# Performance work log

Hardware: AMD Instinct MI355X
Metric: run time of the kernel (lower is better)

## Reference

```python
import jax, jax.numpy as jnp
import numpy as np


def reference(x, phi, sigma, M_phi_plus, M_phi_minus, M_u, padded_sl):
    """STU forward: spectral FFT convolution + autoregressive input term.

    x:   (B, L, D) input sequence
    phi: (L, K) time-domain spectral filters (top-K Hankel eigenvectors);
         V = rfft(phi, n=padded_sl) matches the module's precomputed V.
    sigma: (K,) Hankel eigenvalues
    M_phi_plus/minus: (K, D, D) per-filter projections
    M_u: (k_u, D, D) AR-on-input matrices
    """
    B, L, D = x.shape
    K = sigma.shape[0]
    n = padded_sl  # FFT length for causal linear convolution

    # Alternating-sign trick for the 'minus' featurization:
    # sum_j (-1)^j phi_j u_{t-j} = (-1)^t * conv(phi, sgn*u)_t
    sgn = jnp.where(jnp.arange(L) % 2 == 0, 1.0, -1.0).astype(x.dtype)[None, :, None]  # (1,L,1)

    V = jnp.fft.rfft(phi, n=n, axis=0)                       # (n//2+1, K) complex
    U = jnp.fft.rfft(jnp.stack([x, x * sgn], axis=-1), n=n, axis=1)  # (B, n//2+1, D, 2)
    prod = V[None, :, :, None, None] * U[:, :, None, :, :]    # (B, n//2+1, K, D, 2)
    conv = jnp.fft.irfft(prod, n=n, axis=1)[:, :L]            # (B, L, K, D, 2) causal conv
    U_plus = conv[..., 0]
    U_minus = conv[..., 1] * sgn[..., None]                   # undo sign on output side

    # Fold sigma^{1/4} scaling into the projection matrices.
    sig4 = (sigma ** 0.25).astype(x.dtype)[:, None, None]     # (K,1,1)
    spectral = (
        jnp.einsum('blkd,kdo->blo', U_plus, M_phi_plus * sig4)
        + jnp.einsum('blkd,kdo->blo', U_minus, M_phi_minus * sig4)
    )

    # compute_ar_u: y_t += sum_{i=0}^{k_u-1} x_{t-i} @ M_u[i]  (use_ar_u=True)
    ar_u = jnp.einsum('bld,do->blo', x, M_u[0])
    for i in range(1, M_u.shape[0]):  # small fixed depth k_u=3
        x_shift = jnp.pad(x, ((0, 0), (i, 0), (0, 0)))[:, :L]
        ar_u = ar_u + jnp.einsum('bld,do->blo', x_shift, M_u[i])

    # use_ar_y=False branch; dropout=0 (identity)
    return spectral + ar_u


def setup_inputs() -> dict:
    key = jax.random.key(0)
    ks = jax.random.split(key, 6)
    B, L, D, K, KU, N = 1, 2048, 768, 16, 3, 4096
    x = jax.random.normal(ks[0], (B, L, D), jnp.float32)
    phi = jax.random.normal(ks[1], (L, K), jnp.float32) / np.sqrt(L).astype(np.float32)
    sigma = jax.random.uniform(ks[2], (K,), jnp.float32, 0.1, 1.0)
    M_phi_plus = jax.random.normal(ks[3], (K, D, D), jnp.float32) * 0.02
    M_phi_minus = jax.random.normal(ks[4], (K, D, D), jnp.float32) * 0.02
    M_u = jax.random.normal(ks[5], (KU, D, D), jnp.float32) * 0.02
    return {"x": x, "phi": phi, "sigma": sigma, "M_phi_plus": M_phi_plus,
            "M_phi_minus": M_phi_minus, "M_u": M_u, "padded_sl": N}
```

## Files before the change

### kernel.cpp

```cpp
#include <hip/hip_runtime.h>

typedef __attribute__((ext_vector_type(8))) short bf16x8;
typedef __attribute__((ext_vector_type(4))) float f32x4;

#define SL 2048
#define DM 768
#define NCH 32
#define MSPEC 24576
#define MTOT  26880

#define SPLITK 10
#define KSLICE 2688
#define NT 42
#define NITER 21

__device__ __forceinline__ short f2bf(float f) {
  unsigned u = __builtin_bit_cast(unsigned, f);
  u = (u + 0x7FFFu + ((u >> 16) & 1u)) >> 16;
  return (short)u;
}

__device__ __forceinline__ void gload16(const short* g, short* l) {
  __builtin_amdgcn_global_load_lds(
      (const __attribute__((address_space(1))) void*)g,
      (__attribute__((address_space(3))) void*)l, 16, 0, 0);
}


__global__ __launch_bounds__(256) void k_zero(float4* out) {
  out[blockIdx.x * 256 + threadIdx.x] = float4{0.f, 0.f, 0.f, 0.f};
}

__global__ __launch_bounds__(256) void k_prep_xT(const float* __restrict__ x,
                                                 short* __restrict__ xT) {
  __shared__ short tile[64][65];
  const int d0 = blockIdx.x * 64, l0 = blockIdx.y * 64;
  const int t = threadIdx.x;
#pragma unroll
  for (int rr = 0; rr < 16; ++rr) {
    int ll = rr * 4 + (t >> 6), dl = t & 63;
    tile[ll][dl] = f2bf(x[(size_t)(l0 + ll) * DM + d0 + dl]);
  }
  __syncthreads();
#pragma unroll
  for (int rr = 0; rr < 16; ++rr) {
    int dl = rr * 4 + (t >> 6), ll = t & 63;
    xT[(size_t)(d0 + dl) * SL + l0 + ll] = tile[ll][dl];
  }
}

__global__ __launch_bounds__(256) void k_prep_ar(const float* __restrict__ x,
                                                 short* __restrict__ U) {
  int id = blockIdx.x * 256 + threadIdx.x;
  int l = id / DM, d = id - l * DM;
#pragma unroll
  for (int i = 0; i < 3; ++i) {
    short v = 0;
    if (l >= i) v = f2bf(x[(size_t)(l - i) * DM + d]);
    U[(size_t)l * MTOT + MSPEC + i * DM + d] = v;
  }
}

__global__ __launch_bounds__(256) void k_prep_T(const float* __restrict__ phi,
                                                short* __restrict__ Tmat) {
  int idx = blockIdx.x * 256 + threadIdx.x;
  int b = idx & 127, a = (idx >> 7) & 127, dlag = (idx >> 14) & 15, c = idx >> 18;
  int j = dlag * 128 + a - b;
  short v = 0;
  if (j >= 0) {
    float p = phi[j * 16 + (c & 15)];
    if (c >= 16 && (j & 1)) p = -p;
    v = f2bf(p);
  }
  Tmat[idx] = v;
}

__global__ __launch_bounds__(256) void k_prep_M(const float* __restrict__ Mp,
                                                const float* __restrict__ Mm,
                                                const float* __restrict__ Mu,
                                                const float* __restrict__ sigma,
                                                short* __restrict__ McatT) {
  __shared__ short tile[64][65];
  const int m0 = blockIdx.x * 64, o0 = blockIdx.y * 64;
  const int t = threadIdx.x;
#pragma unroll
  for (int rr = 0; rr < 16; ++rr) {
    int ml = rr * 4 + (t >> 6), ol = t & 63;
    int m = m0 + ml, o = o0 + ol;
    float v;
    if (m < MSPEC) {
      int c = m / DM, d = m - c * DM;
      int k = c & 15;
      float s4 = sqrtf(sqrtf(sigma[k]));
      if (c < 16) v = Mp[((size_t)c * DM + d) * DM + o] * s4;
      else        v = Mm[((size_t)(c - 16) * DM + d) * DM + o] * s4;
    } else {
      int mm = m - MSPEC;
      int i = mm / DM, d = mm - i * DM;
      v = Mu[((size_t)i * DM + d) * DM + o];
    }
    tile[ml][ol] = f2bf(v);
  }
  __syncthreads();
#pragma unroll
  for (int rr = 0; rr < 16; ++rr) {
    int ol = rr * 4 + (t >> 6), ml = t & 63;
    McatT[(size_t)(o0 + ol) * MTOT + m0 + ml] = tile[ml][ol];
  }
}

__global__ __launch_bounds__(256) void k_gemm1(const short* __restrict__ Tmat,
                                               const short* __restrict__ xT,
                                               short* __restrict__ U) {
  __shared__ __align__(16) short As[2][128 * 32];
  __shared__ __align__(16) short Bs[2][128 * 32];
  const int wid = blockIdx.x;
  const int xcd = wid & 7;
  const int slot = wid >> 3;
  const int c = xcd * 4 + (slot & 3);
  const int dtile = (slot >> 2) % 6;
  const int ib = 15 - (slot >> 2) / 6;
  const int t = threadIdx.x;
  const int lane = t & 63, wave = t >> 6;
  const int wm = (wave >> 1) * 64, wn = (wave & 1) * 64;
  const int lrow = lane & 15, quad = lane >> 4;
  const int l4 = lane >> 2, lq = lane & 3;
  const int r0 = wave * 32 + l4;
  const int swz = (lq ^ ((l4 >> 1) & 3)) * 8;
  const int foff = ((quad ^ ((lrow >> 1) & 3)) << 3);

  f32x4 acc[4][4] = {};
  const short* Abase = Tmat + ((size_t)(c * 16) << 14) + r0 * 128 + swz;
  const short* Bbase = xT + (size_t)dtile * 128 * SL + (size_t)r0 * SL + swz;
  const int nit = 4 * (ib + 1);

  auto stage = [&](int it, int buf) {
    int dlag = it >> 2, kk = it & 3;
    const short* Ad = Abase + ((size_t)dlag << 14) + kk * 32;
    const short* Bd = Bbase + (ib - dlag) * 128 + kk * 32;
    short* lA = &As[buf][wave * 1024 + lane * 8];
    short* lB = &Bs[buf][wave * 1024 + lane * 8];
    gload16(Ad, lA);
    gload16(Ad + 16 * 128, lA + 512);
    gload16(Bd, lB);
    gload16(Bd + 16 * SL, lB + 512);
  };

  stage(0, 0);
  int cur = 0;
  for (int it = 0; it < nit; ++it) {
    __syncthreads();
    if (it + 1 < nit) stage(it + 1, cur ^ 1);
    bf16x8 af[4], bfr[4];
#pragma unroll
    for (int im = 0; im < 4; ++im)
      af[im] = *reinterpret_cast<const bf16x8*>(&As[cur][(wm + im * 16 + lrow) * 32 + foff]);
#pragma unroll
    for (int in = 0; in < 4; ++in)
      bfr[in] = *reinterpret_cast<const bf16x8*>(&Bs[cur][(wn + in * 16 + lrow) * 32 + foff]);
#pragma unroll
    for (int im = 0; im < 4; ++im)
#pragma unroll
      for (int in = 0; in < 4; ++in)
        acc[im][in] = __builtin_amdgcn_mfma_f32_16x16x32_bf16(af[im], bfr[in], acc[im][in], 0, 0, 0);
    cur ^= 1;
  }
  const int l0 = ib * 128, colbase = c * DM + dtile * 128;
#pragma unroll
  for (int im = 0; im < 4; ++im)
#pragma unroll
    for (int in = 0; in < 4; ++in)
#pragma unroll
      for (int r4 = 0; r4 < 4; ++r4) {
        int row = wm + im * 16 + quad * 4 + r4;
        int col = wn + in * 16 + lrow;
        U[(size_t)(l0 + row) * MTOT + colbase + col] = f2bf(acc[im][in][r4]);
      }
}


#define LDSREADS(BUF, KS, MQ)                                                   \
    _Pragma("unroll")                                                           \
    for (int q_ = 0; q_ < 4; ++q_)                                              \
      af_[q_] = *reinterpret_cast<const bf16x8*>(                               \
          &As[BUF][KS][wm1][((MQ) * 64 + q_ * 16 + lrow) * 32 + foff]);         \
    if ((MQ) == 0) {                                                            \
      _Pragma("unroll")                                                         \
      for (int i_ = 0; i_ < 4; ++i_)                                            \
        bf_[i_] = *reinterpret_cast<const bf16x8*>(                             \
            &Bs[BUF][KS][hB][(rB0 + i_ * 16 + lrow) * 32 + foff]);              \
    }

#define DOMFMA(MQ)                                                              \
    _Pragma("unroll")                                                           \
    for (int q_ = 0; q_ < 4; ++q_)                                              \
      _Pragma("unroll")                                                         \
      for (int i_ = 0; i_ < 4; ++i_)                                            \
        acc[(MQ) * 4 + q_][i_] = __builtin_amdgcn_mfma_f32_16x16x32_bf16(       \
            af_[q_], bf_[i_], acc[(MQ) * 4 + q_][i_], 0, 0, 0)

#define STA(SBUF, SKS, SKT) do { int kt_ = (SKT); if (kt_ < NT) {               \
    const short* g_ = Abase + kt_ * 64 + (SKS) * 32;                            \
    gload16(g_, &As[SBUF][SKS][0][t8]);                                         \
    gload16(g_ + (size_t)128 * MTOT, &As[SBUF][SKS][1][t8]); } } while (0)

#define STB(SBUF, SKS, SKT) do { int kt_ = (SKT); if (kt_ < NT) {               \
    const short* g_ = Bbase + kt_ * 64 + (SKS) * 32;                            \
    gload16(g_, &Bs[SBUF][SKS][0][t8]);                                         \
    gload16(g_ + (size_t)128 * MTOT, &Bs[SBUF][SKS][1][t8]); } } while (0)

#define PHASE(BUF, KS, MQ, VMODE, STG) do {                                     \
    asm volatile("" ::: "memory");            \
    bf16x8 af_[4];                                                              \
    if ((VMODE) == 1) asm volatile("s_waitcnt vmcnt(6)" ::: "memory");          \
    if ((VMODE) == 2) {                                                         \
      if (j < NITER - 1) asm volatile("s_waitcnt vmcnt(6)" ::: "memory");       \
      else               asm volatile("s_waitcnt vmcnt(0)" ::: "memory");       \
    }                                                                           \
    if ((VMODE) == 0) { LDSREADS(BUF, KS, MQ) }                                 \
    STG;                                                                        \
    __builtin_amdgcn_s_barrier();                                               \
    asm volatile("" ::: "memory");                                              \
    if ((VMODE) != 0) { LDSREADS(BUF, KS, MQ) }                                 \
    asm volatile("s_waitcnt lgkmcnt(0)" ::: "memory");                          \
    __builtin_amdgcn_sched_barrier(0);                                          \
    __builtin_amdgcn_s_setprio(1);                                              \
    DOMFMA(MQ);                                                                 \
    __builtin_amdgcn_s_setprio(0);                                              \
    __builtin_amdgcn_s_barrier();                                               \
  } while (0)

__global__ __launch_bounds__(512, 2) void k_gemm2_8p(const short* __restrict__ U,
                                                     const short* __restrict__ McatT,
                                                     float* __restrict__ out) {
  __shared__ __align__(16) short As[2][2][2][4096];
  __shared__ __align__(16) short Bs[2][2][2][4096];
  const int bid = blockIdx.x;
  const int tile = bid % 24, kc = bid / 24;
  const int mt = tile & 7, nt_ = tile >> 3;
  const int m0 = mt * 256, o0 = nt_ * 256;
  const int kbase = kc * KSLICE;
  const int t = threadIdx.x;
  const int lane = t & 63, wave = t >> 6;
  const int wm1 = wave >> 2;
  const int hB = (wave & 3) >> 1;
  const int rB0 = (wave & 1) * 64;
  const int lrow = lane & 15, quad = lane >> 4;
  const int foff = (quad ^ ((lrow >> 1) & 3)) << 3;
  const int r = t >> 2;
  const int cswz = ((t & 3) ^ ((r >> 1) & 3)) << 3;
  const int t8 = t * 8;

  const short* Abase = U     + (size_t)(m0 + r) * MTOT + kbase + cswz;
  const short* Bbase = McatT + (size_t)(o0 + r) * MTOT + kbase + cswz;

  f32x4 acc[8][4] = {};

  STB(0, 0, 0); STA(0, 0, 0); STB(0, 1, 0); STA(0, 1, 0);
  STB(1, 0, 1); STA(1, 0, 1); STB(1, 1, 1);

  for (int j = 0; j < NITER; ++j) {
    bf16x8 bf_[4];
    PHASE(0, 0, 0, 1, STA(1, 1, 2 * j + 1));
    PHASE(0, 0, 1, 0, STB(0, 0, 2 * j + 2));
    PHASE(0, 1, 0, 0, STA(0, 0, 2 * j + 2));
    PHASE(0, 1, 1, 0, STB(0, 1, 2 * j + 2));
    PHASE(1, 0, 0, 2, STA(0, 1, 2 * j + 2));
    PHASE(1, 0, 1, 0, STB(1, 0, 2 * j + 3));
    PHASE(1, 1, 0, 0, STA(1, 0, 2 * j + 3));
    PHASE(1, 1, 1, 0, STB(1, 1, 2 * j + 3));
  }

  const int wm128 = (wave >> 2) * 128, wn64 = (wave & 3) * 64;
#pragma unroll
  for (int im = 0; im < 8; ++im)
#pragma unroll
    for (int in = 0; in < 4; ++in)
#pragma unroll
      for (int r4 = 0; r4 < 4; ++r4) {
        int row = m0 + wm128 + im * 16 + quad * 4 + r4;
        int col = o0 + wn64 + in * 16 + lrow;
        atomicAdd(&out[(size_t)row * DM + col], acc[im][in][r4]);
      }
}

extern "C" void kernel_launch(void* const* d_in, const int* in_sizes, int n_in,
                              void* d_out, int out_size, void* d_ws, size_t ws_size,
                              hipStream_t stream) {
  (void)in_sizes; (void)n_in; (void)out_size; (void)ws_size;
  const float* x     = (const float*)d_in[0];
  const float* phi   = (const float*)d_in[1];
  const float* sigma = (const float*)d_in[2];
  const float* Mp    = (const float*)d_in[3];
  const float* Mm    = (const float*)d_in[4];
  const float* Mu    = (const float*)d_in[5];
  float* out = (float*)d_out;
  char* ws = (char*)d_ws;

  short* U     = (short*)(ws);
  short* Tmat  = (short*)(ws + 110100480);
  short* xT    = (short*)(ws + 126877696);
  short* McatT = (short*)(ws + 130023424);

  k_zero<<<dim3(1536), dim3(256), 0, stream>>>((float4*)out);
  k_prep_xT<<<dim3(12, 32), dim3(256), 0, stream>>>(x, xT);
  k_prep_ar<<<dim3(6144), dim3(256), 0, stream>>>(x, U);
  k_prep_T<<<dim3(32768), dim3(256), 0, stream>>>(phi, Tmat);
  k_prep_M<<<dim3(420, 12), dim3(256), 0, stream>>>(Mp, Mm, Mu, sigma, McatT);
  k_gemm1<<<dim3(3072), dim3(256), 0, stream>>>(Tmat, xT, U);
  k_gemm2_8p<<<dim3(240), dim3(512), 0, stream>>>(U, McatT, out);
}
```

Before: 419.5 us.

## Retile Toeplitz conv GEMM to 256x256 8-phase pipeline; add split-K partial reduce

Replaces the 128x128 Toeplitz-convolution GEMM with a 256x256-tile, 512-thread kernel that reuses the 8-phase software-pipelined schedule of the projection GEMM. It adds a zero block to Tmat so the causal lag lookups near the diagonal can read zeros instead of branching. When the workspace is large enough, the split-K projection GEMM writes per-slice partials and a separate reduction kernel sums them, replacing the zero-fill and float atomics. The cost is extra workspace and extra memory traffic for the partials, plus coarser load balance in the triangular first GEMM.

```diff
diff --git a/kernel.cpp b/kernel.cpp
--- a/kernel.cpp
+++ b/kernel.cpp
@@ -11,8 +11,15 @@
 
 #define SPLITK 10
 #define KSLICE 2688
-#define NT 42
-#define NITER 21
+#define NT2 42
+#define NITER2 21
+
+#define WS_U      0
+#define WS_TMAT   110100480ULL
+#define WS_XT     126910464ULL
+#define WS_MCAT   130056192ULL
+#define WS_PART   171343872ULL
+#define WS_NEED   234258432ULL
 
 __device__ __forceinline__ short f2bf(float f) {
   unsigned u = __builtin_bit_cast(unsigned, f);
@@ -64,7 +71,9 @@
 __global__ __launch_bounds__(256) void k_prep_T(const float* __restrict__ phi,
                                                 short* __restrict__ Tmat) {
   int idx = blockIdx.x * 256 + threadIdx.x;
-  int b = idx & 127, a = (idx >> 7) & 127, dlag = (idx >> 14) & 15, c = idx >> 18;
+  int c = idx >> 18;
+  if (c >= 32) { Tmat[idx] = 0; return; }
+  int b = idx & 127, a = (idx >> 7) & 127, dlag = (idx >> 14) & 15;
   int j = dlag * 128 + a - b;
   short v = 0;
   if (j >= 0) {
@@ -109,75 +118,6 @@
   }
 }
 
-__global__ __launch_bounds__(256) void k_gemm1(const short* __restrict__ Tmat,
-                                               const short* __restrict__ xT,
-                                               short* __restrict__ U) {
-  __shared__ __align__(16) short As[2][128 * 32];
-  __shared__ __align__(16) short Bs[2][128 * 32];
-  const int wid = blockIdx.x;
-  const int xcd = wid & 7;
-  const int slot = wid >> 3;
-  const int c = xcd * 4 + (slot & 3);
-  const int dtile = (slot >> 2) % 6;
-  const int ib = 15 - (slot >> 2) / 6;
-  const int t = threadIdx.x;
-  const int lane = t & 63, wave = t >> 6;
-  const int wm = (wave >> 1) * 64, wn = (wave & 1) * 64;
-  const int lrow = lane & 15, quad = lane >> 4;
-  const int l4 = lane >> 2, lq = lane & 3;
-  const int r0 = wave * 32 + l4;
-  const int swz = (lq ^ ((l4 >> 1) & 3)) * 8;
-  const int foff = ((quad ^ ((lrow >> 1) & 3)) << 3);
-
-  f32x4 acc[4][4] = {};
-  const short* Abase = Tmat + ((size_t)(c * 16) << 14) + r0 * 128 + swz;
-  const short* Bbase = xT + (size_t)dtile * 128 * SL + (size_t)r0 * SL + swz;
-  const int nit = 4 * (ib + 1);
-
-  auto stage = [&](int it, int buf) {
-    int dlag = it >> 2, kk = it & 3;
-    const short* Ad = Abase + ((size_t)dlag << 14) + kk * 32;
-    const short* Bd = Bbase + (ib - dlag) * 128 + kk * 32;
-    short* lA = &As[buf][wave * 1024 + lane * 8];
-    short* lB = &Bs[buf][wave * 1024 + lane * 8];
-    gload16(Ad, lA);
-    gload16(Ad + 16 * 128, lA + 512);
-    gload16(Bd, lB);
-    gload16(Bd + 16 * SL, lB + 512);
-  };
-
-  stage(0, 0);
-  int cur = 0;
-  for (int it = 0; it < nit; ++it) {
-    __syncthreads();
-    if (it + 1 < nit) stage(it + 1, cur ^ 1);
-    bf16x8 af[4], bfr[4];
-#pragma unroll
-    for (int im = 0; im < 4; ++im)
-      af[im] = *reinterpret_cast<const bf16x8*>(&As[cur][(wm + im * 16 + lrow) * 32 + foff]);
-#pragma unroll
-    for (int in = 0; in < 4; ++in)
-      bfr[in] = *reinterpret_cast<const bf16x8*>(&Bs[cur][(wn + in * 16 + lrow) * 32 + foff]);
-#pragma unroll
-    for (int im = 0; im < 4; ++im)
-#pragma unroll
-      for (int in = 0; in < 4; ++in)
-        acc[im][in] = __builtin_amdgcn_mfma_f32_16x16x32_bf16(af[im], bfr[in], acc[im][in], 0, 0, 0);
-    cur ^= 1;
-  }
-  const int l0 = ib * 128, colbase = c * DM + dtile * 128;
-#pragma unroll
-  for (int im = 0; im < 4; ++im)
-#pragma unroll
-    for (int in = 0; in < 4; ++in)
-#pragma unroll
-      for (int r4 = 0; r4 < 4; ++r4) {
-        int row = wm + im * 16 + quad * 4 + r4;
-        int col = wn + in * 16 + lrow;
-        U[(size_t)(l0 + row) * MTOT + colbase + col] = f2bf(acc[im][in][r4]);
-      }
-}
-
 
 #define LDSREADS(BUF, KS, MQ)                                                   \
     _Pragma("unroll")                                                           \
@@ -199,23 +139,13 @@
         acc[(MQ) * 4 + q_][i_] = __builtin_amdgcn_mfma_f32_16x16x32_bf16(       \
             af_[q_], bf_[i_], acc[(MQ) * 4 + q_][i_], 0, 0, 0)
 
-#define STA(SBUF, SKS, SKT) do { int kt_ = (SKT); if (kt_ < NT) {               \
-    const short* g_ = Abase + kt_ * 64 + (SKS) * 32;                            \
-    gload16(g_, &As[SBUF][SKS][0][t8]);                                         \
-    gload16(g_ + (size_t)128 * MTOT, &As[SBUF][SKS][1][t8]); } } while (0)
-
-#define STB(SBUF, SKS, SKT) do { int kt_ = (SKT); if (kt_ < NT) {               \
-    const short* g_ = Bbase + kt_ * 64 + (SKS) * 32;                            \
-    gload16(g_, &Bs[SBUF][SKS][0][t8]);                                         \
-    gload16(g_ + (size_t)128 * MTOT, &Bs[SBUF][SKS][1][t8]); } } while (0)
-
 #define PHASE(BUF, KS, MQ, VMODE, STG) do {                                     \
     asm volatile("" ::: "memory");            \
     bf16x8 af_[4];                                                              \
     if ((VMODE) == 1) asm volatile("s_waitcnt vmcnt(6)" ::: "memory");          \
     if ((VMODE) == 2) {                                                         \
-      if (j < NITER - 1) asm volatile("s_waitcnt vmcnt(6)" ::: "memory");       \
-      else               asm volatile("s_waitcnt vmcnt(0)" ::: "memory");       \
+      if (j < nIterM1) asm volatile("s_waitcnt vmcnt(6)" ::: "memory");         \
+      else             asm volatile("s_waitcnt vmcnt(0)" ::: "memory");         \
     }                                                                           \
     if ((VMODE) == 0) { LDSREADS(BUF, KS, MQ) }                                 \
     STG;                                                                        \
@@ -230,9 +160,99 @@
     __builtin_amdgcn_s_barrier();                                               \
   } while (0)
 
+
+#define STA1(SBUF, SKS, SKT) do { int kt_ = (SKT); if (kt_ < nT) {              \
+    int kch_ = kt_ * 64 + (SKS) * 32;                                           \
+    int kb_ = kch_ >> 7, bo_ = kch_ & 127;                                      \
+    int dl_ = 2 * rt - kb_;                                                     \
+    const short* g0_ = (dl_ >= 0) ? (Tc + ((size_t)dl_ << 14) + bo_)            \
+                                  : (Tz + bo_);                                 \
+    const short* g1_ = Tc + ((size_t)(dl_ + 1) << 14) + bo_;                    \
+    gload16(g0_, &As[SBUF][SKS][0][t8]);                                        \
+    gload16(g1_, &As[SBUF][SKS][1][t8]); } } while (0)
+
+#define STB1(SBUF, SKS, SKT) do { int kt_ = (SKT); if (kt_ < nT) {              \
+    const short* g_ = Bb + kt_ * 64 + (SKS) * 32;                               \
+    gload16(g_, &Bs[SBUF][SKS][0][t8]);                                         \
+    gload16(g_ + (size_t)128 * SL, &Bs[SBUF][SKS][1][t8]); } } while (0)
+
+__global__ __launch_bounds__(512, 2) void k_gemm1_8p(const short* __restrict__ Tmat,
+                                                     const short* __restrict__ xT,
+                                                     short* __restrict__ U) {
+  __shared__ __align__(16) short As[2][2][2][4096];
+  __shared__ __align__(16) short Bs[2][2][2][4096];
+  const int bid = blockIdx.x;
+  const int xcd = bid & 7;
+  const int slot = bid >> 3;
+  const int c = xcd * 4 + (slot & 3);
+  const int q = slot >> 2;
+  const int ct = q % 3;
+  const int rt = 7 - q / 3;
+  const int nT = 4 * (rt + 1);
+  const int nIter = 2 * (rt + 1);
+  const int nIterM1 = nIter - 1;
+  const int t = threadIdx.x;
+  const int lane = t & 63, wave = t >> 6;
+  const int wm1 = wave >> 2;
+  const int hB = (wave & 3) >> 1;
+  const int rB0 = (wave & 1) * 64;
+  const int lrow = lane & 15, quad = lane >> 4;
+  const int foff = (quad ^ ((lrow >> 1) & 3)) << 3;
+  const int r = t >> 2;
+  const int cswz = ((t & 3) ^ ((r >> 1) & 3)) << 3;
+  const int t8 = t * 8;
+
+  const short* Tc = Tmat + ((size_t)(c * 16) << 14) + r * 128 + cswz;
+  const short* Tz = Tmat + ((size_t)512 << 14) + r * 128 + cswz;
+  const short* Bb = xT + (size_t)(ct * 256 + r) * SL + cswz;
+
+  f32x4 acc[8][4] = {};
+
+  STB1(0, 0, 0); STA1(0, 0, 0); STB1(0, 1, 0); STA1(0, 1, 0);
+  STB1(1, 0, 1); STA1(1, 0, 1); STB1(1, 1, 1);
+
+  for (int j = 0; j < nIter; ++j) {
+    bf16x8 bf_[4];
+    PHASE(0, 0, 0, 1, STA1(1, 1, 2 * j + 1));
+    PHASE(0, 0, 1, 0, STB1(0, 0, 2 * j + 2));
+    PHASE(0, 1, 0, 0, STA1(0, 0, 2 * j + 2));
+    PHASE(0, 1, 1, 0, STB1(0, 1, 2 * j + 2));
+    PHASE(1, 0, 0, 2, STA1(0, 1, 2 * j + 2));
+    PHASE(1, 0, 1, 0, STB1(1, 0, 2 * j + 3));
+    PHASE(1, 1, 0, 0, STA1(1, 0, 2 * j + 3));
+    PHASE(1, 1, 1, 0, STB1(1, 1, 2 * j + 3));
+  }
+
+  const int wm128 = (wave >> 2) * 128, wn64 = (wave & 3) * 64;
+  const int l0 = rt * 256, colbase = c * DM + ct * 256;
+#pragma unroll
+  for (int im = 0; im < 8; ++im)
+#pragma unroll
+    for (int in = 0; in < 4; ++in)
+#pragma unroll
+      for (int r4 = 0; r4 < 4; ++r4) {
+        int row = l0 + wm128 + im * 16 + quad * 4 + r4;
+        int col = colbase + wn64 + in * 16 + lrow;
+        U[(size_t)row * MTOT + col] = f2bf(acc[im][in][r4]);
+      }
+}
+
+
+#define STA2(SBUF, SKS, SKT) do { int kt_ = (SKT); if (kt_ < NT2) {             \
+    const short* g_ = Abase + kt_ * 64 + (SKS) * 32;                            \
+    gload16(g_, &As[SBUF][SKS][0][t8]);                                         \
+    gload16(g_ + (size_t)128 * MTOT, &As[SBUF][SKS][1][t8]); } } while (0)
+
+#define STB2(SBUF, SKS, SKT) do { int kt_ = (SKT); if (kt_ < NT2) {             \
+    const short* g_ = Bbase + kt_ * 64 + (SKS) * 32;                            \
+    gload16(g_, &Bs[SBUF][SKS][0][t8]);                                         \
+    gload16(g_ + (size_t)128 * MTOT, &Bs[SBUF][SKS][1][t8]); } } while (0)
+
 __global__ __launch_bounds__(512, 2) void k_gemm2_8p(const short* __restrict__ U,
                                                      const short* __restrict__ McatT,
-                                                     float* __restrict__ out) {
+                                                     float* __restrict__ out,
+                                                     float* __restrict__ part,
+                                                     int use_part) {
   __shared__ __align__(16) short As[2][2][2][4096];
   __shared__ __align__(16) short Bs[2][2][2][4096];
   const int bid = blockIdx.x;
@@ -250,44 +270,71 @@
   const int r = t >> 2;
   const int cswz = ((t & 3) ^ ((r >> 1) & 3)) << 3;
   const int t8 = t * 8;
+  const int nIterM1 = NITER2 - 1;
 
   const short* Abase = U     + (size_t)(m0 + r) * MTOT + kbase + cswz;
   const short* Bbase = McatT + (size_t)(o0 + r) * MTOT + kbase + cswz;
 
   f32x4 acc[8][4] = {};
 
-  STB(0, 0, 0); STA(0, 0, 0); STB(0, 1, 0); STA(0, 1, 0);
-  STB(1, 0, 1); STA(1, 0, 1); STB(1, 1, 1);
-
-  for (int j = 0; j < NITER; ++j) {
+  STB2(0, 0, 0); STA2(0, 0, 0); STB2(0, 1, 0); STA2(0, 1, 0);
+  STB2(1, 0, 1); STA2(1, 0, 1); STB2(1, 1, 1);
+
+  for (int j = 0; j < NITER2; ++j) {
     bf16x8 bf_[4];
-    PHASE(0, 0, 0, 1, STA(1, 1, 2 * j + 1));
-    PHASE(0, 0, 1, 0, STB(0, 0, 2 * j + 2));
-    PHASE(0, 1, 0, 0, STA(0, 0, 2 * j + 2));
-    PHASE(0, 1, 1, 0, STB(0, 1, 2 * j + 2));
-    PHASE(1, 0, 0, 2, STA(0, 1, 2 * j + 2));
-    PHASE(1, 0, 1, 0, STB(1, 0, 2 * j + 3));
-    PHASE(1, 1, 0, 0, STA(1, 0, 2 * j + 3));
-    PHASE(1, 1, 1, 0, STB(1, 1, 2 * j + 3));
+    PHASE(0, 0, 0, 1, STA2(1, 1, 2 * j + 1));
+    PHASE(0, 0, 1, 0, STB2(0, 0, 2 * j + 2));
+    PHASE(0, 1, 0, 0, STA2(0, 0, 2 * j + 2));
+    PHASE(0, 1, 1, 0, STB2(0, 1, 2 * j + 2));
+    PHASE(1, 0, 0, 2, STA2(0, 1, 2 * j + 2));
+    PHASE(1, 0, 1, 0, STB2(1, 0, 2 * j + 3));
+    PHASE(1, 1, 0, 0, STA2(1, 0, 2 * j + 3));
+    PHASE(1, 1, 1, 0, STB2(1, 1, 2 * j + 3));
   }
 
   const int wm128 = (wave >> 2) * 128, wn64 = (wave & 3) * 64;
-#pragma unroll
-  for (int im = 0; im < 8; ++im)
-#pragma unroll
-    for (int in = 0; in < 4; ++in)
-#pragma unroll
-      for (int r4 = 0; r4 < 4; ++r4) {
-        int row = m0 + wm128 + im * 16 + quad * 4 + r4;
-        int col = o0 + wn64 + in * 16 + lrow;
-        atomicAdd(&out[(size_t)row * DM + col], acc[im][in][r4]);
-      }
+  if (use_part) {
+    float* dst = part + (size_t)kc * (2048 * 768);
+#pragma unroll
+    for (int im = 0; im < 8; ++im)
+#pragma unroll
+      for (int in = 0; in < 4; ++in)
+#pragma unroll
+        for (int r4 = 0; r4 < 4; ++r4) {
+          int row = m0 + wm128 + im * 16 + quad * 4 + r4;
+          int col = o0 + wn64 + in * 16 + lrow;
+          dst[(size_t)row * DM + col] = acc[im][in][r4];
+        }
+  } else {
+#pragma unroll
+    for (int im = 0; im < 8; ++im)
+#pragma unroll
+      for (int in = 0; in < 4; ++in)
+#pragma unroll
+        for (int r4 = 0; r4 < 4; ++r4) {
+          int row = m0 + wm128 + im * 16 + quad * 4 + r4;
+          int col = o0 + wn64 + in * 16 + lrow;
+          atomicAdd(&out[(size_t)row * DM + col], acc[im][in][r4]);
+        }
+  }
+}
+
+__global__ __launch_bounds__(256) void k_reduce(const float4* __restrict__ part,
+                                                float4* __restrict__ out) {
+  int i = blockIdx.x * 256 + threadIdx.x;
+  float4 s = part[i];
+#pragma unroll
+  for (int k = 1; k < SPLITK; ++k) {
+    float4 v = part[(size_t)k * 393216 + i];
+    s.x += v.x; s.y += v.y; s.z += v.z; s.w += v.w;
+  }
+  out[i] = s;
 }
 
 extern "C" void kernel_launch(void* const* d_in, const int* in_sizes, int n_in,
                               void* d_out, int out_size, void* d_ws, size_t ws_size,
                               hipStream_t stream) {
-  (void)in_sizes; (void)n_in; (void)out_size; (void)ws_size;
+  (void)in_sizes; (void)n_in; (void)out_size;
   const float* x     = (const float*)d_in[0];
   const float* phi   = (const float*)d_in[1];
   const float* sigma = (const float*)d_in[2];
@@ -297,16 +344,21 @@
   float* out = (float*)d_out;
   char* ws = (char*)d_ws;
 
-  short* U     = (short*)(ws);
-  short* Tmat  = (short*)(ws + 110100480);
-  short* xT    = (short*)(ws + 126877696);
-  short* McatT = (short*)(ws + 130023424);
-
-  k_zero<<<dim3(1536), dim3(256), 0, stream>>>((float4*)out);
+  short* U     = (short*)(ws + WS_U);
+  short* Tmat  = (short*)(ws + WS_TMAT);
+  short* xT    = (short*)(ws + WS_XT);
+  short* McatT = (short*)(ws + WS_MCAT);
+  float* Wpart = (float*)(ws + WS_PART);
+  const int use_part = ws_size >= WS_NEED ? 1 : 0;
+
+  if (!use_part)
+    k_zero<<<dim3(1536), dim3(256), 0, stream>>>((float4*)out);
   k_prep_xT<<<dim3(12, 32), dim3(256), 0, stream>>>(x, xT);
   k_prep_ar<<<dim3(6144), dim3(256), 0, stream>>>(x, U);
-  k_prep_T<<<dim3(32768), dim3(256), 0, stream>>>(phi, Tmat);
+  k_prep_T<<<dim3(32832), dim3(256), 0, stream>>>(phi, Tmat);
   k_prep_M<<<dim3(420, 12), dim3(256), 0, stream>>>(Mp, Mm, Mu, sigma, McatT);
-  k_gemm1<<<dim3(3072), dim3(256), 0, stream>>>(Tmat, xT, U);
-  k_gemm2_8p<<<dim3(240), dim3(512), 0, stream>>>(U, McatT, out);
-}
+  k_gemm1_8p<<<dim3(768), dim3(512), 0, stream>>>(Tmat, xT, U);
+  k_gemm2_8p<<<dim3(240), dim3(512), 0, stream>>>(U, McatT, out, Wpart, use_part);
+  if (use_part)
+    k_reduce<<<dim3(1536), dim3(256), 0, stream>>>((const float4*)Wpart, (float4*)out);
+}
```

Result: faster. 386.0 us (-8.0%).
